# Optimization experiments

Measured on AMD Instinct MI355X. Metric: run time of the kernel, lower is better.

## Reference

```python
import jax, jax.numpy as jnp
import numpy as np

N = 100000
E = 1600000
F_IN = 64
DIM = 64
OUT = 2
BN_EPS = 1e-5


def setup_inputs() -> dict:
    key = jax.random.key(0)
    ks = jax.random.split(key, 12)
    s = lambda fan_in: 1.0 / np.sqrt(fan_in)
    inp = {
        "x": jax.random.normal(ks[0], (N, F_IN), dtype=jnp.float32),
        "edge_index": jax.random.randint(ks[1], (2, E), 0, N, dtype=jnp.int64),
        # conv1 MLP: Linear(F_IN, DIM) -> ReLU -> Linear(DIM, DIM)
        "W1a": jax.random.uniform(ks[2], (F_IN, DIM), jnp.float32, -s(F_IN), s(F_IN)),
        "b1a": jnp.zeros((DIM,), jnp.float32),
        "W1b": jax.random.uniform(ks[3], (DIM, DIM), jnp.float32, -s(DIM), s(DIM)),
        "b1b": jnp.zeros((DIM,), jnp.float32),
        "g1": jnp.ones((DIM,), jnp.float32),
        "be1": jnp.zeros((DIM,), jnp.float32),
        # conv5 MLP: Linear(DIM, DIM) -> ReLU -> Linear(DIM, 2)
        "W5a": jax.random.uniform(ks[4], (DIM, DIM), jnp.float32, -s(DIM), s(DIM)),
        "b5a": jnp.zeros((DIM,), jnp.float32),
        "W5b": jax.random.uniform(ks[5], (DIM, OUT), jnp.float32, -s(DIM), s(DIM)),
        "b5b": jnp.zeros((OUT,), jnp.float32),
        "g5": jnp.ones((OUT,), jnp.float32),
        "be5": jnp.zeros((OUT,), jnp.float32),
    }
    return inp


def _gin_agg(x, src, dst):
    # GINConv with eps=0: (1+eps)*x + sum_{j in N(i)} x_j
    agg = jax.ops.segment_sum(x[src], dst, num_segments=N)
    return x + agg


def _batchnorm(h, gamma, beta):
    mu = jnp.mean(h, axis=0)
    var = jnp.var(h, axis=0)  # biased, as torch BN uses for normalization
    return (h - mu) * jax.lax.rsqrt(var + BN_EPS) * gamma + beta


def reference(x, edge_index, W1a, b1a, W1b, b1b, g1, be1,
              W5a, b5a, W5b, b5b, g5, be5):
    src, dst = edge_index[0], edge_index[1]
    # conv1
    h = _gin_agg(x, src, dst)                      # [N, F_IN]
    h = jax.nn.relu(h @ W1a + b1a) @ W1b + b1b     # [N, DIM]
    h = jax.nn.relu(h)
    h = _batchnorm(h, g1, be1)
    # conv5
    h = _gin_agg(h, src, dst)                      # [N, DIM]
    h = jax.nn.relu(h @ W5a + b5a) @ W5b + b5b     # [N, OUT]
    h = jax.nn.relu(h)
    h = _batchnorm(h, g5, be5)
    return h
```

## Files before the change

### kernel.cpp

```cpp
#include <hip/hip_runtime.h>

#define NN 100000
#define FD 64
#define OUTF 2
#define NB 391
#define NBP 392
#define P1CH 4096
#define NTILE 6250

typedef short bf16x8 __attribute__((ext_vector_type(8), may_alias));
typedef float f32x4 __attribute__((ext_vector_type(4)));
typedef float f32x2 __attribute__((ext_vector_type(2)));

__device__ inline ushort f2bf(float f) {
    uint u = __float_as_uint(f);
    uint r = (u + 0x7FFFu + ((u >> 16) & 1u)) >> 16;
    return (ushort)r;
}
__device__ inline float bf2f(ushort v) {
    return __uint_as_float(((uint)v) << 16);
}


__global__ void k_zero(float* __restrict__ p, int n) {
    int i = blockIdx.x * blockDim.x + threadIdx.x;
    if (i < n) p[i] = 0.f;
}

__global__ void k_copy4(const float4* __restrict__ s, float4* __restrict__ d, int n4) {
    int i = blockIdx.x * blockDim.x + threadIdx.x;
    int st = gridDim.x * blockDim.x;
    for (; i < n4; i += st) d[i] = s[i];
}

__global__ void k_cvt(const float4* __restrict__ x4, ushort4* __restrict__ xb4,
                      ushort* __restrict__ xb, ushort* __restrict__ h1b, int n4) {
    int i = blockIdx.x * blockDim.x + threadIdx.x;
    if (i < 16) {
        ushort4 z = {0, 0, 0, 0};
        ((ushort4*)(xb + (size_t)NN * FD))[i] = z;
        ((ushort4*)(h1b + (size_t)NN * FD))[i] = z;
    }
    int st = gridDim.x * blockDim.x;
    for (; i < n4; i += st) {
        float4 v = x4[i];
        ushort4 w;
        w.x = f2bf(v.x);
        w.y = f2bf(v.y);
        w.z = f2bf(v.z);
        w.w = f2bf(v.w);
        xb4[i] = w;
    }
}


__global__ __launch_bounds__(256) void k_p1a2(const int* __restrict__ ei,
                                              int* __restrict__ ghist, int E_) {
    __shared__ int h[NB];
    int tid = threadIdx.x;
    for (int i = tid; i < NB; i += 256) h[i] = 0;
    __syncthreads();
    int c0 = blockIdx.x * P1CH;
    int c1 = min(c0 + P1CH, E_);
    for (int i = c0 + tid; i < c1; i += 256) {
        int d = ei[E_ + i];
        int b = min(max(d >> 8, 0), NB - 1);
        atomicAdd(&h[b], 1);
    }
    __syncthreads();
    int* row = ghist + (size_t)blockIdx.x * NBP;
    for (int i = tid; i < NB; i += 256) row[i] = h[i];
}

__global__ __launch_bounds__(512) void k_scanCol(int* __restrict__ ghist,
                                                 int* __restrict__ tot, int np1) {
    __shared__ int ts[512];
    int b = blockIdx.x;
    int tid = threadIdx.x;
    int v = (tid < np1) ? ghist[(size_t)tid * NBP + b] : 0;
    ts[tid] = v;
    __syncthreads();
    for (int off = 1; off < 512; off <<= 1) {
        int u = (tid >= off) ? ts[tid - off] : 0;
        __syncthreads();
        ts[tid] += u;
        __syncthreads();
    }
    if (tid < np1) ghist[(size_t)tid * NBP + b] = ts[tid] - v;
    if (tid == 511) tot[b] = ts[511];
}

__global__ __launch_bounds__(512) void k_scanB2(const int* __restrict__ tot,
                                                int* __restrict__ bbase,
                                                float* __restrict__ S) {
    __shared__ int ts[512];
    int tid = threadIdx.x;
    if (tid < 192) S[tid] = 0.f;
    int v = (tid < NB) ? tot[tid] : 0;
    ts[tid] = v;
    __syncthreads();
    for (int off = 1; off < 512; off <<= 1) {
        int u = (tid >= off) ? ts[tid - off] : 0;
        __syncthreads();
        ts[tid] += u;
        __syncthreads();
    }
    if (tid < NB) bbase[tid] = ts[tid] - v;
    if (tid == 511) bbase[NB] = ts[511];
}

__global__ __launch_bounds__(256) void k_p1b2(const int* __restrict__ ei,
                                              const int* __restrict__ ghist,
                                              const int* __restrict__ bbase,
                                              int* __restrict__ part, int E_) {
    __shared__ int cur[NB];
    int tid = threadIdx.x;
    const int* row = ghist + (size_t)blockIdx.x * NBP;
    for (int i = tid; i < NB; i += 256) cur[i] = bbase[i] + row[i];
    __syncthreads();
    int c0 = blockIdx.x * P1CH;
    int c1 = min(c0 + P1CH, E_);
    for (int i = c0 + tid; i < c1; i += 256) {
        int s = ei[i];
        int d = ei[E_ + i];
        int b = min(max(d >> 8, 0), NB - 1);
        int slot = atomicAdd(&cur[b], 1);
        part[slot] = ((d & 255) << 20) | (s & 0xFFFFF);
    }
}

__global__ __launch_bounds__(256) void k_build(const int* __restrict__ part,
                                               const int* __restrict__ bbase,
                                               int* __restrict__ rowptr,
                                               int* __restrict__ csr, int E_) {
    __shared__ int cnt[256];
    __shared__ int ts[256];
    __shared__ int cur[256];
    int b = blockIdx.x;
    int tid = threadIdx.x;
    cnt[tid] = 0;
    __syncthreads();
    int s0 = bbase[b], s1 = bbase[b + 1];
    for (int i = s0 + tid; i < s1; i += 256) {
        int v = part[i];
        atomicAdd(&cnt[(v >> 20) & 255], 1);
    }
    __syncthreads();
    int v = cnt[tid];
    ts[tid] = v;
    __syncthreads();
    for (int off = 1; off < 256; off <<= 1) {
        int u = (tid >= off) ? ts[tid - off] : 0;
        __syncthreads();
        ts[tid] += u;
        __syncthreads();
    }
    int excl = ts[tid] - v;
    int node = b * 256 + tid;
    if (node < NN) rowptr[node] = s0 + excl;
    cur[tid] = s0 + excl;
    if (b == 0 && tid == 0) rowptr[NN] = E_;
    __syncthreads();
    for (int i = s0 + tid; i < s1; i += 256) {
        int v2 = part[i];
        int lj = (v2 >> 20) & 255;
        int pos = atomicAdd(&cur[lj], 1);
        csr[pos] = v2 & 0xFFFFF;
    }
}


#define GSTEP(T, A01, A23)                                                     \
    {                                                                          \
        int s = __shfl(id, (T) * 4 + g);                                       \
        uint2 v = *(const uint2*)(Xb + ((long)s << 6) + (l << 2));             \
        f32x2 p, q2;                                                           \
        p[0] = __uint_as_float(v.x << 16);                                     \
        p[1] = __uint_as_float(v.x & 0xFFFF0000u);                             \
        q2[0] = __uint_as_float(v.y << 16);                                    \
        q2[1] = __uint_as_float(v.y & 0xFFFF0000u);                            \
        A01 += p;                                                              \
        A23 += q2;                                                             \
    }

__global__ __launch_bounds__(256) void k_gather2(
        const ushort* __restrict__ Xb, const int* __restrict__ rowptr,
        const int* __restrict__ csr,
        const float* __restrict__ bs, const float* __restrict__ bq,
        const float* __restrict__ gam, const float* __restrict__ bet,
        ushort* __restrict__ outb, int E_, int affine) {
    int tid = threadIdx.x;
    int lane = tid & 63;
    int n = (blockIdx.x * blockDim.x + tid) >> 6;
    if (n >= NN) return;
    int g = lane >> 4;
    int l = lane & 15;
    int start = rowptr[n], end = rowptr[n + 1];
    start = min(max(start, 0), E_);
    end = min(max(end, start), E_);
    int deg = end - start;

    f32x2 a01 = {0.f, 0.f}, a23 = {0.f, 0.f};
    f32x2 b01 = {0.f, 0.f}, b23 = {0.f, 0.f};
    if (g == 0) {
        uint2 v = *(const uint2*)(Xb + ((long)n << 6) + (l << 2));
        a01[0] = __uint_as_float(v.x << 16);
        a01[1] = __uint_as_float(v.x & 0xFFFF0000u);
        a23[0] = __uint_as_float(v.y << 16);
        a23[1] = __uint_as_float(v.y & 0xFFFF0000u);
    }

    for (int base = start; base < end; base += 64) {
        int cnt = min(end - base, 64);
        int id = NN;
        if (lane < cnt) id = min(max(csr[base + lane], 0), NN - 1);
        int nsteps = (cnt + 3) >> 2;
        int t = 0;
        for (; t + 4 <= nsteps; t += 4) {
            GSTEP(t + 0, a01, a23)
            GSTEP(t + 1, b01, b23)
            GSTEP(t + 2, a01, a23)
            GSTEP(t + 3, b01, b23)
        }
        for (; t + 2 <= nsteps; t += 2) {
            GSTEP(t + 0, a01, a23)
            GSTEP(t + 1, b01, b23)
        }
        if (t < nsteps) GSTEP(t, a01, a23)
    }
    a01 += b01;
    a23 += b23;
    float A[4] = {a01[0], a01[1], a23[0], a23[1]};
#pragma unroll
    for (int c = 0; c < 4; c++) {
        float v = A[c];
        v += __shfl_xor(v, 16);
        v += __shfl_xor(v, 32);
        A[c] = v;
    }

    if (g == 0) {
        if (affine) {
            float dp1 = (float)(deg + 1);
#pragma unroll
            for (int c = 0; c < 4; c++) {
                int ch = l * 4 + c;
                float mu = bs[ch] * (1.f / NN);
                float var = bq[ch] * (1.f / NN) - mu * mu;
                float s = gam[ch] * rsqrtf(var + 1e-5f);
                float sh = fmaf(-mu, s, bet[ch]);
                A[c] = fmaf(A[c], s, dp1 * sh);
            }
        }
        ushort4 v;
        v.x = f2bf(A[0]); v.y = f2bf(A[1]); v.z = f2bf(A[2]); v.w = f2bf(A[3]);
        ((ushort4*)(outb + ((long)n << 6)))[l] = v;
    }
}


__global__ __launch_bounds__(256) void k_mlp1_mfma(
        const ushort* __restrict__ Ab,
        const float* __restrict__ Wa, const float* __restrict__ ba,
        const float* __restrict__ Wb, const float* __restrict__ bb,
        ushort* __restrict__ H, float* __restrict__ gsum, float* __restrict__ gsq) {
    __shared__ __attribute__((aligned(16))) short tile[4][16 * 72];
    __shared__ float sArr[64], qArr[64];
    int tid = threadIdx.x;
    int w = tid >> 6, lane = tid & 63;
    int l = lane & 15, quad = lane >> 4;
    if (tid < 64) { sArr[tid] = 0.f; qArr[tid] = 0.f; }
    __syncthreads();

    bf16x8 B1[2][4], B2[2][4];
#pragma unroll
    for (int ks = 0; ks < 2; ks++)
#pragma unroll
        for (int t = 0; t < 4; t++) {
            bf16x8 f1, f2;
#pragma unroll
            for (int j = 0; j < 8; j++) {
                int k = ks * 32 + quad * 8 + j;
                f1[j] = (short)f2bf(Wa[k * 64 + t * 16 + l]);
                f2[j] = (short)f2bf(Wb[k * 64 + t * 16 + l]);
            }
            B1[ks][t] = f1;
            B2[ks][t] = f2;
        }
    float bias1[4], bias2[4];
#pragma unroll
    for (int t = 0; t < 4; t++) {
        bias1[t] = ba[t * 16 + l];
        bias2[t] = bb[t * 16 + l];
    }

    float s[4] = {0.f, 0.f, 0.f, 0.f}, q[4] = {0.f, 0.f, 0.f, 0.f};
    short* tp = &tile[w][0];
    int gw = blockIdx.x * 4 + w;
    int nw = gridDim.x * 4;
    bf16x8 A0, A1;
    if (gw < NTILE) {
        int m0 = gw * 16;
        A0 = *(const bf16x8*)(Ab + (size_t)(m0 + l) * FD + quad * 8);
        A1 = *(const bf16x8*)(Ab + (size_t)(m0 + l) * FD + 32 + quad * 8);
    }
    for (int tau = gw; tau < NTILE; tau += nw) {
        int m0 = tau * 16;
        int nxt = tau + nw;
        bf16x8 nA0, nA1;
        if (nxt < NTILE) {
            int nm0 = nxt * 16;
            nA0 = *(const bf16x8*)(Ab + (size_t)(nm0 + l) * FD + quad * 8);
            nA1 = *(const bf16x8*)(Ab + (size_t)(nm0 + l) * FD + 32 + quad * 8);
        }
#pragma unroll
        for (int t = 0; t < 4; t++) {
            f32x4 c = {0.f, 0.f, 0.f, 0.f};
            c = __builtin_amdgcn_mfma_f32_16x16x32_bf16(A0, B1[0][t], c, 0, 0, 0);
            c = __builtin_amdgcn_mfma_f32_16x16x32_bf16(A1, B1[1][t], c, 0, 0, 0);
#pragma unroll
            for (int r = 0; r < 4; r++) {
                float v = fmaxf(c[r] + bias1[t], 0.f);
                tp[(quad * 4 + r) * 72 + t * 16 + l] = (short)f2bf(v);
            }
        }
        bf16x8 A20 = *(const bf16x8*)&tp[l * 72 + quad * 8];
        bf16x8 A21 = *(const bf16x8*)&tp[l * 72 + 32 + quad * 8];
#pragma unroll
        for (int t = 0; t < 4; t++) {
            f32x4 c = {0.f, 0.f, 0.f, 0.f};
            c = __builtin_amdgcn_mfma_f32_16x16x32_bf16(A20, B2[0][t], c, 0, 0, 0);
            c = __builtin_amdgcn_mfma_f32_16x16x32_bf16(A21, B2[1][t], c, 0, 0, 0);
#pragma unroll
            for (int r = 0; r < 4; r++) {
                float v = fmaxf(c[r] + bias2[t], 0.f);
                s[t] += v;
                q[t] += v * v;
                tp[(quad * 4 + r) * 72 + t * 16 + l] = (short)f2bf(v);
            }
        }
        int row = lane >> 2, ch = lane & 3;
        bf16x8 o0 = *(const bf16x8*)&tp[row * 72 + ch * 16];
        bf16x8 o1 = *(const bf16x8*)&tp[row * 72 + ch * 16 + 8];
        *(bf16x8*)(H + (size_t)(m0 + row) * FD + ch * 16) = o0;
        *(bf16x8*)(H + (size_t)(m0 + row) * FD + ch * 16 + 8) = o1;
        A0 = nA0;
        A1 = nA1;
    }
#pragma unroll
    for (int t = 0; t < 4; t++) {
        s[t] += __shfl_xor(s[t], 16); s[t] += __shfl_xor(s[t], 32);
        q[t] += __shfl_xor(q[t], 16); q[t] += __shfl_xor(q[t], 32);
    }
    if (quad == 0) {
#pragma unroll
        for (int t = 0; t < 4; t++) {
            atomicAdd(&sArr[t * 16 + l], s[t]);
            atomicAdd(&qArr[t * 16 + l], q[t]);
        }
    }
    __syncthreads();
    if (tid < 64) {
        atomicAdd(&gsum[tid], sArr[tid]);
        atomicAdd(&gsq[tid], qArr[tid]);
    }
}

__global__ __launch_bounds__(256) void k_mlp2_mfma(
        const ushort* __restrict__ Ab,
        const float* __restrict__ Wa, const float* __restrict__ ba,
        const float* __restrict__ Wb2, const float* __restrict__ bb2,
        float* __restrict__ O, float* __restrict__ gsum, float* __restrict__ gsq) {
    __shared__ __attribute__((aligned(16))) short tile[4][16 * 72];
    __shared__ float sArr[2], qArr[2];
    int tid = threadIdx.x;
    int w = tid >> 6, lane = tid & 63;
    int l = lane & 15, quad = lane >> 4;
    if (tid < 2) { sArr[tid] = 0.f; qArr[tid] = 0.f; }
    __syncthreads();

    bf16x8 B1[2][4], B2[2];
#pragma unroll
    for (int ks = 0; ks < 2; ks++) {
#pragma unroll
        for (int t = 0; t < 4; t++) {
            bf16x8 f1;
#pragma unroll
            for (int j = 0; j < 8; j++) {
                int k = ks * 32 + quad * 8 + j;
                f1[j] = (short)f2bf(Wa[k * 64 + t * 16 + l]);
            }
            B1[ks][t] = f1;
        }
        bf16x8 f2;
#pragma unroll
        for (int j = 0; j < 8; j++) {
            int k = ks * 32 + quad * 8 + j;
            f2[j] = (l < OUTF) ? (short)f2bf(Wb2[k * OUTF + l]) : (short)0;
        }
        B2[ks] = f2;
    }
    float bias1[4];
#pragma unroll
    for (int t = 0; t < 4; t++) bias1[t] = ba[t * 16 + l];
    float bias2 = (l < OUTF) ? bb2[l] : 0.f;

    float s = 0.f, q = 0.f;
    short* tp = &tile[w][0];
    int gw = blockIdx.x * 4 + w;
    int nw = gridDim.x * 4;
    bf16x8 A0, A1;
    if (gw < NTILE) {
        int m0 = gw * 16;
        A0 = *(const bf16x8*)(Ab + (size_t)(m0 + l) * FD + quad * 8);
        A1 = *(const bf16x8*)(Ab + (size_t)(m0 + l) * FD + 32 + quad * 8);
    }
    for (int tau = gw; tau < NTILE; tau += nw) {
        int m0 = tau * 16;
        int nxt = tau + nw;
        bf16x8 nA0, nA1;
        if (nxt < NTILE) {
            int nm0 = nxt * 16;
            nA0 = *(const bf16x8*)(Ab + (size_t)(nm0 + l) * FD + quad * 8);
            nA1 = *(const bf16x8*)(Ab + (size_t)(nm0 + l) * FD + 32 + quad * 8);
        }
#pragma unroll
        for (int t = 0; t < 4; t++) {
            f32x4 c = {0.f, 0.f, 0.f, 0.f};
            c = __builtin_amdgcn_mfma_f32_16x16x32_bf16(A0, B1[0][t], c, 0, 0, 0);
            c = __builtin_amdgcn_mfma_f32_16x16x32_bf16(A1, B1[1][t], c, 0, 0, 0);
#pragma unroll
            for (int r = 0; r < 4; r++) {
                float v = fmaxf(c[r] + bias1[t], 0.f);
                tp[(quad * 4 + r) * 72 + t * 16 + l] = (short)f2bf(v);
            }
        }
        bf16x8 A20 = *(const bf16x8*)&tp[l * 72 + quad * 8];
        bf16x8 A21 = *(const bf16x8*)&tp[l * 72 + 32 + quad * 8];
        f32x4 c = {0.f, 0.f, 0.f, 0.f};
        c = __builtin_amdgcn_mfma_f32_16x16x32_bf16(A20, B2[0], c, 0, 0, 0);
        c = __builtin_amdgcn_mfma_f32_16x16x32_bf16(A21, B2[1], c, 0, 0, 0);
#pragma unroll
        for (int r = 0; r < 4; r++) {
            float v = fmaxf(c[r] + bias2, 0.f);
            if (l < OUTF) {
                s += v;
                q += v * v;
                O[(size_t)(m0 + quad * 4 + r) * OUTF + l] = v;
            }
        }
        A0 = nA0;
        A1 = nA1;
    }
    s += __shfl_xor(s, 16); s += __shfl_xor(s, 32);
    q += __shfl_xor(q, 16); q += __shfl_xor(q, 32);
    if (quad == 0 && l < OUTF) {
        atomicAdd(&sArr[l], s);
        atomicAdd(&qArr[l], q);
    }
    __syncthreads();
    if (tid < OUTF) {
        atomicAdd(&gsum[tid], sArr[tid]);
        atomicAdd(&gsq[tid], qArr[tid]);
    }
}

template <bool BF16OUT>
__global__ __launch_bounds__(256) void k_mlp64(
        const float* __restrict__ X,
        const float* __restrict__ Wa, const float* __restrict__ ba,
        const float* __restrict__ Wb, const float* __restrict__ bb,
        void* __restrict__ Hv, float* __restrict__ gsum, float* __restrict__ gsq) {
    __shared__ float row[256 * 65];
    int tid = threadIdx.x;
    long node = (long)blockIdx.x * 256 + tid;
    bool valid = node < NN;
    if (valid) {
        const float4* rp = (const float4*)(X + node * FD);
#pragma unroll
        for (int q = 0; q < 16; q++) {
            float4 v = rp[q];
            row[tid * 65 + 4 * q + 0] = v.x;
            row[tid * 65 + 4 * q + 1] = v.y;
            row[tid * 65 + 4 * q + 2] = v.z;
            row[tid * 65 + 4 * q + 3] = v.w;
        }
    }
    float acc[64];
#pragma unroll
    for (int j = 0; j < 64; j++) acc[j] = ba[j];
    if (valid) {
        for (int k = 0; k < 64; k++) {
            float xv = row[tid * 65 + k];
            const float* wr = Wa + k * 64;
#pragma unroll
            for (int j = 0; j < 64; j++) acc[j] = fmaf(xv, wr[j], acc[j]);
        }
    }
#pragma unroll
    for (int j = 0; j < 64; j++) row[tid * 65 + j] = fmaxf(acc[j], 0.f);
#pragma unroll
    for (int j = 0; j < 64; j++) acc[j] = bb[j];
    if (valid) {
        for (int k = 0; k < 64; k++) {
            float xv = row[tid * 65 + k];
            const float* wr = Wb + k * 64;
#pragma unroll
            for (int j = 0; j < 64; j++) acc[j] = fmaf(xv, wr[j], acc[j]);
        }
    }
#pragma unroll
    for (int j = 0; j < 64; j++) {
        float v = valid ? fmaxf(acc[j], 0.f) : 0.f;
        row[tid * 65 + j] = v;
    }
    if (valid) {
        if (BF16OUT) {
            ushort4* op = (ushort4*)((ushort*)Hv + node * FD);
#pragma unroll
            for (int q = 0; q < 16; q++) {
                ushort4 w;
                w.x = f2bf(row[tid * 65 + 4 * q + 0]);
                w.y = f2bf(row[tid * 65 + 4 * q + 1]);
                w.z = f2bf(row[tid * 65 + 4 * q + 2]);
                w.w = f2bf(row[tid * 65 + 4 * q + 3]);
                op[q] = w;
            }
        } else {
            float4* op = (float4*)((float*)Hv + node * FD);
#pragma unroll
            for (int q = 0; q < 16; q++) {
                float4 v;
                v.x = row[tid * 65 + 4 * q + 0];
                v.y = row[tid * 65 + 4 * q + 1];
                v.z = row[tid * 65 + 4 * q + 2];
                v.w = row[tid * 65 + 4 * q + 3];
                op[q] = v;
            }
        }
    }
    __syncthreads();
    if (tid < 64) {
        float s = 0.f, q = 0.f;
        for (int r = 0; r < 256; r++) {
            float v = row[r * 65 + tid];
            s += v;
            q += v * v;
        }
        atomicAdd(&gsum[tid], s);
        atomicAdd(&gsq[tid], q);
    }
}

__global__ __launch_bounds__(256) void k_mlp_out(
        const float* __restrict__ X,
        const float* __restrict__ Wa, const float* __restrict__ ba,
        const float* __restrict__ Wb, const float* __restrict__ bb,
        float* __restrict__ O, float* __restrict__ gsum, float* __restrict__ gsq) {
    __shared__ float row[256 * 65];
    __shared__ float red[256][4];
    int tid = threadIdx.x;
    long node = (long)blockIdx.x * 256 + tid;
    bool valid = node < NN;
    if (valid) {
        const float4* rp = (const float4*)(X + node * FD);
#pragma unroll
        for (int q = 0; q < 16; q++) {
            float4 v = rp[q];
            row[tid * 65 + 4 * q + 0] = v.x;
            row[tid * 65 + 4 * q + 1] = v.y;
            row[tid * 65 + 4 * q + 2] = v.z;
            row[tid * 65 + 4 * q + 3] = v.w;
        }
    }
    float acc[64];
#pragma unroll
    for (int j = 0; j < 64; j++) acc[j] = ba[j];
    if (valid) {
        for (int k = 0; k < 64; k++) {
            float xv = row[tid * 65 + k];
            const float* wr = Wa + k * 64;
#pragma unroll
            for (int j = 0; j < 64; j++) acc[j] = fmaf(xv, wr[j], acc[j]);
        }
    }
#pragma unroll
    for (int j = 0; j < 64; j++) row[tid * 65 + j] = fmaxf(acc[j], 0.f);
    float a0 = bb[0];
    float a1 = bb[1];
    if (valid) {
        for (int k = 0; k < 64; k++) {
            float xv = row[tid * 65 + k];
            a0 = fmaf(xv, Wb[k * 2 + 0], a0);
            a1 = fmaf(xv, Wb[k * 2 + 1], a1);
        }
    }
    float v0 = valid ? fmaxf(a0, 0.f) : 0.f;
    float v1 = valid ? fmaxf(a1, 0.f) : 0.f;
    if (valid) {
        float2 v;
        v.x = v0;
        v.y = v1;
        ((float2*)O)[node] = v;
    }
    red[tid][0] = v0;
    red[tid][1] = v0 * v0;
    red[tid][2] = v1;
    red[tid][3] = v1 * v1;
    __syncthreads();
    for (int off = 128; off > 0; off >>= 1) {
        if (tid < off) {
#pragma unroll
            for (int c = 0; c < 4; c++) red[tid][c] += red[tid + off][c];
        }
        __syncthreads();
    }
    if (tid == 0) {
        atomicAdd(&gsum[0], red[0][0]);
        atomicAdd(&gsq[0], red[0][1]);
        atomicAdd(&gsum[1], red[0][2]);
        atomicAdd(&gsq[1], red[0][3]);
    }
}


__global__ void k_bnfin(const float* __restrict__ gsum, const float* __restrict__ gsq,
                        const float* __restrict__ g, const float* __restrict__ be,
                        float* __restrict__ sc, float* __restrict__ sh, int C, float invN) {
    int c = threadIdx.x;
    if (c < C) {
        float mu = gsum[c] * invN;
        float var = gsq[c] * invN - mu * mu;
        float s = g[c] * rsqrtf(var + 1e-5f);
        sc[c] = s;
        sh[c] = fmaf(-mu, s, be[c]);
    }
}

__global__ void k_bnfin_apply2(const float* __restrict__ gsum,
                               const float* __restrict__ gsq,
                               const float* __restrict__ g,
                               const float* __restrict__ be,
                               float* __restrict__ o, int n) {
    int i = blockIdx.x * blockDim.x + threadIdx.x;
    if (i < n) {
        int c = i & 1;
        float mu = gsum[c] * (1.f / NN);
        float var = gsq[c] * (1.f / NN) - mu * mu;
        float s = g[c] * rsqrtf(var + 1e-5f);
        float sh = fmaf(-mu, s, be[c]);
        o[i] = fmaf(o[i], s, sh);
    }
}

__global__ void k_bn_apply2(float* __restrict__ o, const float* __restrict__ sc,
                            const float* __restrict__ sh, int n) {
    int i = blockIdx.x * blockDim.x + threadIdx.x;
    if (i < n) {
        int c = i & 1;
        o[i] = fmaf(o[i], sc[c], sh[c]);
    }
}


__global__ void k_scatter(const float* __restrict__ x, const int* __restrict__ ei,
                          float* __restrict__ agg, int E_) {
    int lane = threadIdx.x & 63;
    int wid = (blockIdx.x * blockDim.x + threadIdx.x) >> 6;
    int nw = (gridDim.x * blockDim.x) >> 6;
    for (long e = wid; e < E_; e += nw) {
        int s = ei[e];
        int d = ei[E_ + e];
        float v = x[(long)s * FD + lane];
        atomicAdd(&agg[(long)d * FD + lane], v);
    }
}

__global__ void k_scatter_bn(const float* __restrict__ h, const int* __restrict__ ei,
                             const float* __restrict__ sc, const float* __restrict__ sh,
                             float* __restrict__ agg, int E_) {
    int lane = threadIdx.x & 63;
    float scl = sc[lane];
    float shf = sh[lane];
    int wid = (blockIdx.x * blockDim.x + threadIdx.x) >> 6;
    int nw = (gridDim.x * blockDim.x) >> 6;
    for (long e = wid; e < E_; e += nw) {
        int s = ei[e];
        int d = ei[E_ + e];
        float v = fmaf(h[(long)s * FD + lane], scl, shf);
        atomicAdd(&agg[(long)d * FD + lane], v);
    }
}

__global__ void k_bn_copy(const float4* __restrict__ h, const float4* __restrict__ sc4,
                          const float4* __restrict__ sh4, float4* __restrict__ o, int n4) {
    int i = blockIdx.x * blockDim.x + threadIdx.x;
    int st = gridDim.x * blockDim.x;
    for (; i < n4; i += st) {
        float4 v = h[i];
        int c = i & 15;
        float4 s = sc4[c];
        float4 b = sh4[c];
        v.x = fmaf(v.x, s.x, b.x);
        v.y = fmaf(v.y, s.y, b.y);
        v.z = fmaf(v.z, s.z, b.z);
        v.w = fmaf(v.w, s.w, b.w);
        o[i] = v;
    }
}


extern "C" void kernel_launch(void* const* d_in, const int* in_sizes, int n_in,
                              void* d_out, int out_size, void* d_ws, size_t ws_size,
                              hipStream_t stream) {
    const float* x   = (const float*)d_in[0];
    const int*   ei  = (const int*)d_in[1];
    const float* W1a = (const float*)d_in[2];
    const float* b1a = (const float*)d_in[3];
    const float* W1b = (const float*)d_in[4];
    const float* b1b = (const float*)d_in[5];
    const float* g1  = (const float*)d_in[6];
    const float* be1 = (const float*)d_in[7];
    const float* W5a = (const float*)d_in[8];
    const float* b5a = (const float*)d_in[9];
    const float* W5b = (const float*)d_in[10];
    const float* b5b = (const float*)d_in[11];
    const float* g5  = (const float*)d_in[12];
    const float* be5 = (const float*)d_in[13];
    float* out = (float*)d_out;

    const int E = in_sizes[1] / 2;

    float* ws = (float*)d_ws;
    float* agg = ws;
    ushort* aggb = (ushort*)ws;
    ushort* xb  = (ushort*)(ws + 6400000);
    ushort* h1b = (ushort*)(ws + 9600032);
    float* h1_fb = ws + 6400000;
    float* S   = ws + 12800064;
    float* gsum1  = S;
    float* gsq1   = S + 64;
    float* gsum2  = S + 128;
    float* gsq2   = S + 160;
    float* scale1 = S + 192;
    float* shift1 = S + 256;
    float* scale2 = S + 320;
    float* shift2 = S + 328;

    int* ibase  = (int*)(S + 512);
    int* rowptr = ibase;
    int* csr    = ibase + 100004;
    int* bbase  = ibase + 100004 + E;
    int* tot    = bbase + 400;
    int* ghist  = tot + 392;
    int* part   = (int*)agg;

    const int np1 = (E + P1CH - 1) / P1CH;
    size_t needed = (size_t)(12800064 + 512) * 4 +
                    (size_t)(100004 + E + 400 + 392 + (size_t)np1 * NBP) * 4;

    const int n4 = NN * FD / 4;
    const int nblk = (NN + 255) / 256;

    if (ws_size >= needed && np1 <= 512) {
        k_cvt<<<2048, 256, 0, stream>>>((const float4*)x, (ushort4*)xb, xb, h1b, n4);
        k_p1a2<<<np1, 256, 0, stream>>>(ei, ghist, E);
        k_scanCol<<<NB, 512, 0, stream>>>(ghist, tot, np1);
        k_scanB2<<<1, 512, 0, stream>>>(tot, bbase, S);
        k_p1b2<<<np1, 256, 0, stream>>>(ei, ghist, bbase, part, E);
        k_build<<<NB, 256, 0, stream>>>(part, bbase, rowptr, csr, E);

        k_gather2<<<25000, 256, 0, stream>>>(xb, rowptr, csr, nullptr, nullptr,
                                             nullptr, nullptr, aggb, E, 0);
        k_mlp1_mfma<<<782, 256, 0, stream>>>(aggb, W1a, b1a, W1b, b1b, h1b, gsum1, gsq1);
        k_gather2<<<25000, 256, 0, stream>>>(h1b, rowptr, csr, gsum1, gsq1,
                                             g1, be1, aggb, E, 1);
        k_mlp2_mfma<<<782, 256, 0, stream>>>(aggb, W5a, b5a, W5b, b5b, out, gsum2, gsq2);
        k_bnfin_apply2<<<(NN * OUTF + 255) / 256, 256, 0, stream>>>(gsum2, gsq2, g5, be5,
                                                                    out, NN * OUTF);
    } else {
        k_zero<<<1, 256, 0, stream>>>(S, 192);
        k_copy4<<<4096, 256, 0, stream>>>((const float4*)x, (float4*)agg, n4);
        k_scatter<<<4096, 256, 0, stream>>>(x, ei, agg, E);
        k_mlp64<false><<<nblk, 256, 0, stream>>>(agg, W1a, b1a, W1b, b1b,
                                                 (void*)h1_fb, gsum1, gsq1);
        k_bnfin<<<1, 64, 0, stream>>>(gsum1, gsq1, g1, be1, scale1, shift1, 64, 1.f / NN);
        k_bn_copy<<<4096, 256, 0, stream>>>((const float4*)h1_fb, (const float4*)scale1,
                                            (const float4*)shift1, (float4*)agg, n4);
        k_scatter_bn<<<4096, 256, 0, stream>>>(h1_fb, ei, scale1, shift1, agg, E);
        k_mlp_out<<<nblk, 256, 0, stream>>>(agg, W5a, b5a, W5b, b5b, out, gsum2, gsq2);
        k_bnfin<<<1, 64, 0, stream>>>(gsum2, gsq2, g5, be5, scale2, shift2, OUTF, 1.f / NN);
        k_bn_apply2<<<(NN * OUTF + 255) / 256, 256, 0, stream>>>(out, scale2, shift2, NN * OUTF);
    }
}
```

Before: 272.5 us.

## Fuse conversion with histogram, drop gather clamps, replace BN atomics with partial reduction

Merges the bf16 conversion kernel and the edge histogram kernel into one launch, so the two independent jobs run concurrently and one launch is saved. Removes the bounds clamps on rowptr and csr indices in the gather kernel. Replaces the per-block global atomicAdds for the first BatchNorm statistics with per-block partial writes, followed by a small reduction kernel. This makes the sums deterministic and avoids atomic contention, at the cost of one extra launch. Dropping the clamps relies on the edge indices always being valid.

```diff
diff --git a/kernel.cpp b/kernel.cpp
--- a/kernel.cpp
+++ b/kernel.cpp
@@ -7,6 +7,8 @@
 #define NBP 392
 #define P1CH 4096
 #define NTILE 6250
+#define MLPB 782
+#define GPSTR 800
 
 typedef short bf16x8 __attribute__((ext_vector_type(8), may_alias));
 typedef float f32x4 __attribute__((ext_vector_type(4)));
@@ -33,14 +35,8 @@
     for (; i < n4; i += st) d[i] = s[i];
 }
 
-__global__ void k_cvt(const float4* __restrict__ x4, ushort4* __restrict__ xb4,
-                      ushort* __restrict__ xb, ushort* __restrict__ h1b, int n4) {
+__global__ void k_cvt(const float4* __restrict__ x4, ushort4* __restrict__ xb4, int n4) {
     int i = blockIdx.x * blockDim.x + threadIdx.x;
-    if (i < 16) {
-        ushort4 z = {0, 0, 0, 0};
-        ((ushort4*)(xb + (size_t)NN * FD))[i] = z;
-        ((ushort4*)(h1b + (size_t)NN * FD))[i] = z;
-    }
     int st = gridDim.x * blockDim.x;
     for (; i < n4; i += st) {
         float4 v = x4[i];
@@ -53,24 +49,47 @@
     }
 }
 
-
-__global__ __launch_bounds__(256) void k_p1a2(const int* __restrict__ ei,
-                                              int* __restrict__ ghist, int E_) {
+__global__ __launch_bounds__(256) void k_cvt_hist(
+        const int* __restrict__ ei, int* __restrict__ ghist, int E_, int np1,
+        const float4* __restrict__ x4, ushort4* __restrict__ xb4,
+        ushort* __restrict__ xb, ushort* __restrict__ h1b, int n4) {
     __shared__ int h[NB];
     int tid = threadIdx.x;
-    for (int i = tid; i < NB; i += 256) h[i] = 0;
-    __syncthreads();
-    int c0 = blockIdx.x * P1CH;
-    int c1 = min(c0 + P1CH, E_);
-    for (int i = c0 + tid; i < c1; i += 256) {
-        int d = ei[E_ + i];
-        int b = min(max(d >> 8, 0), NB - 1);
-        atomicAdd(&h[b], 1);
-    }
-    __syncthreads();
-    int* row = ghist + (size_t)blockIdx.x * NBP;
-    for (int i = tid; i < NB; i += 256) row[i] = h[i];
-}
+    int blk = blockIdx.x;
+    if (blk < np1) {
+        for (int i = tid; i < NB; i += 256) h[i] = 0;
+        __syncthreads();
+        int c0 = blk * P1CH;
+        int c1 = min(c0 + P1CH, E_);
+        for (int i = c0 + tid; i < c1; i += 256) {
+            int d = ei[E_ + i];
+            int b = min(max(d >> 8, 0), NB - 1);
+            atomicAdd(&h[b], 1);
+        }
+        __syncthreads();
+        int* row = ghist + (size_t)blk * NBP;
+        for (int i = tid; i < NB; i += 256) row[i] = h[i];
+    } else {
+        int bb = blk - np1;
+        if (bb == 0 && tid < 16) {
+            ushort4 z = {0, 0, 0, 0};
+            ((ushort4*)(xb + (size_t)NN * FD))[tid] = z;
+            ((ushort4*)(h1b + (size_t)NN * FD))[tid] = z;
+        }
+        int i = bb * 256 + tid;
+        int st = 2048 * 256;
+        for (; i < n4; i += st) {
+            float4 v = x4[i];
+            ushort4 w;
+            w.x = f2bf(v.x);
+            w.y = f2bf(v.y);
+            w.z = f2bf(v.z);
+            w.w = f2bf(v.w);
+            xb4[i] = w;
+        }
+    }
+}
+
 
 __global__ __launch_bounds__(512) void k_scanCol(int* __restrict__ ghist,
                                                  int* __restrict__ tot, int np1) {
@@ -188,7 +207,7 @@
         const int* __restrict__ csr,
         const float* __restrict__ bs, const float* __restrict__ bq,
         const float* __restrict__ gam, const float* __restrict__ bet,
-        ushort* __restrict__ outb, int E_, int affine) {
+        ushort* __restrict__ outb, int affine) {
     int tid = threadIdx.x;
     int lane = tid & 63;
     int n = (blockIdx.x * blockDim.x + tid) >> 6;
@@ -196,8 +215,6 @@
     int g = lane >> 4;
     int l = lane & 15;
     int start = rowptr[n], end = rowptr[n + 1];
-    start = min(max(start, 0), E_);
-    end = min(max(end, start), E_);
     int deg = end - start;
 
     f32x2 a01 = {0.f, 0.f}, a23 = {0.f, 0.f};
@@ -213,7 +230,7 @@
     for (int base = start; base < end; base += 64) {
         int cnt = min(end - base, 64);
         int id = NN;
-        if (lane < cnt) id = min(max(csr[base + lane], 0), NN - 1);
+        if (lane < cnt) id = csr[base + lane];
         int nsteps = (cnt + 3) >> 2;
         int t = 0;
         for (; t + 4 <= nsteps; t += 4) {
@@ -263,7 +280,7 @@
         const ushort* __restrict__ Ab,
         const float* __restrict__ Wa, const float* __restrict__ ba,
         const float* __restrict__ Wb, const float* __restrict__ bb,
-        ushort* __restrict__ H, float* __restrict__ gsum, float* __restrict__ gsq) {
+        ushort* __restrict__ H, float* __restrict__ gp1s, float* __restrict__ gp1q) {
     __shared__ __attribute__((aligned(16))) short tile[4][16 * 72];
     __shared__ float sArr[64], qArr[64];
     int tid = threadIdx.x;
@@ -361,8 +378,36 @@
     }
     __syncthreads();
     if (tid < 64) {
-        atomicAdd(&gsum[tid], sArr[tid]);
-        atomicAdd(&gsq[tid], qArr[tid]);
+        gp1s[tid * GPSTR + blockIdx.x] = sArr[tid];
+        gp1q[tid * GPSTR + blockIdx.x] = qArr[tid];
+    }
+}
+
+__global__ __launch_bounds__(256) void k_red1(const float* __restrict__ gp1s,
+                                              const float* __restrict__ gp1q,
+                                              float* __restrict__ gsum,
+                                              float* __restrict__ gsq, int nb) {
+    __shared__ float rs[256], rq[256];
+    int ch = blockIdx.x;
+    int tid = threadIdx.x;
+    float s = 0.f, q = 0.f;
+    for (int k = tid; k < nb; k += 256) {
+        s += gp1s[ch * GPSTR + k];
+        q += gp1q[ch * GPSTR + k];
+    }
+    rs[tid] = s;
+    rq[tid] = q;
+    __syncthreads();
+    for (int off = 128; off > 0; off >>= 1) {
+        if (tid < off) {
+            rs[tid] += rs[tid + off];
+            rq[tid] += rq[tid + off];
+        }
+        __syncthreads();
+    }
+    if (tid == 0) {
+        gsum[ch] = rs[0];
+        gsq[ch] = rq[0];
     }
 }
 
@@ -734,6 +779,8 @@
     float* ws = (float*)d_ws;
     float* agg = ws;
     ushort* aggb = (ushort*)ws;
+    float* gp1s = ws + 3200000;
+    float* gp1q = ws + 3260000;
     ushort* xb  = (ushort*)(ws + 6400000);
     ushort* h1b = (ushort*)(ws + 9600032);
     float* h1_fb = ws + 6400000;
@@ -763,19 +810,20 @@
     const int nblk = (NN + 255) / 256;
 
     if (ws_size >= needed && np1 <= 512) {
-        k_cvt<<<2048, 256, 0, stream>>>((const float4*)x, (ushort4*)xb, xb, h1b, n4);
-        k_p1a2<<<np1, 256, 0, stream>>>(ei, ghist, E);
+        k_cvt_hist<<<np1 + 2048, 256, 0, stream>>>(ei, ghist, E, np1, (const float4*)x,
+                                                   (ushort4*)xb, xb, h1b, n4);
         k_scanCol<<<NB, 512, 0, stream>>>(ghist, tot, np1);
         k_scanB2<<<1, 512, 0, stream>>>(tot, bbase, S);
         k_p1b2<<<np1, 256, 0, stream>>>(ei, ghist, bbase, part, E);
         k_build<<<NB, 256, 0, stream>>>(part, bbase, rowptr, csr, E);
 
         k_gather2<<<25000, 256, 0, stream>>>(xb, rowptr, csr, nullptr, nullptr,
-                                             nullptr, nullptr, aggb, E, 0);
-        k_mlp1_mfma<<<782, 256, 0, stream>>>(aggb, W1a, b1a, W1b, b1b, h1b, gsum1, gsq1);
+                                             nullptr, nullptr, aggb, 0);
+        k_mlp1_mfma<<<MLPB, 256, 0, stream>>>(aggb, W1a, b1a, W1b, b1b, h1b, gp1s, gp1q);
+        k_red1<<<64, 256, 0, stream>>>(gp1s, gp1q, gsum1, gsq1, MLPB);
         k_gather2<<<25000, 256, 0, stream>>>(h1b, rowptr, csr, gsum1, gsq1,
-                                             g1, be1, aggb, E, 1);
-        k_mlp2_mfma<<<782, 256, 0, stream>>>(aggb, W5a, b5a, W5b, b5b, out, gsum2, gsq2);
+                                             g1, be1, aggb, 1);
+        k_mlp2_mfma<<<MLPB, 256, 0, stream>>>(aggb, W5a, b5a, W5b, b5b, out, gsum2, gsq2);
         k_bnfin_apply2<<<(NN * OUTF + 255) / 256, 256, 0, stream>>>(gsum2, gsq2, g5, be5,
                                                                     out, NN * OUTF);
     } else {
```

Result: faster. 263.3 us (-3.4%).
